# Kernel optimization log

Measured on AMD Instinct MI355X. Metric: run time of the kernel, lower is better.

Reference implementation:

```python
import jax, jax.numpy as jnp
import numpy as np

NUM_LAYERS = 3


def setup_inputs() -> dict:
    key = jax.random.key(0)
    ks = jax.random.split(key, 12)
    N, E, D_IN, D, ED = 50000, 800000, 6, 64, 4
    return {
        "x": jax.random.normal(ks[0], (N, D_IN), dtype=jnp.float32),
        "edge_index": jax.random.randint(ks[1], (2, E), 0, N, dtype=jnp.int64),
        "edge_attr": jax.random.normal(ks[2], (E, ED), dtype=jnp.float32),
        "z_soft": jax.random.uniform(ks[3], (E, ED), dtype=jnp.float32),
        "W_nt": jax.random.normal(ks[4], (D, D_IN), dtype=jnp.float32) * 0.1,
        "b_nt": jax.random.normal(ks[5], (D,), dtype=jnp.float32) * 0.1,
        "weight": jax.random.normal(ks[6], (NUM_LAYERS, D, D), dtype=jnp.float32) * 0.1,
        "W_ih": jax.random.normal(ks[7], (3 * D, D), dtype=jnp.float32) * 0.1,
        "W_hh": jax.random.normal(ks[8], (3 * D, D), dtype=jnp.float32) * 0.1,
        "b_ih": jax.random.normal(ks[9], (3 * D,), dtype=jnp.float32) * 0.1,
        "b_hh": jax.random.normal(ks[10], (3 * D,), dtype=jnp.float32) * 0.1,
    }


def gru_cell(m, h, W_ih, W_hh, b_ih, b_hh):
    # PyTorch GRUCell: gates ordered (r, z, n)
    gi = m @ W_ih.T + b_ih
    gh = h @ W_hh.T + b_hh
    i_r, i_z, i_n = jnp.split(gi, 3, axis=-1)
    h_r, h_z, h_n = jnp.split(gh, 3, axis=-1)
    r = jax.nn.sigmoid(i_r + h_r)
    z = jax.nn.sigmoid(i_z + h_z)
    n = jnp.tanh(i_n + r * h_n)
    return (1.0 - z) * n + z * h


def reference(x, edge_index, edge_attr, z_soft, W_nt, b_nt, weight, W_ih, W_hh, b_ih, b_hh):
    # node_transform: Linear + ReLU
    h = jax.nn.relu(x @ W_nt.T + b_nt)  # [N, D]
    # edge_attr gating (faithful to source; unused since edge_weight=None)
    _ = z_soft * edge_attr
    src, dst = edge_index[0], edge_index[1]
    N = h.shape[0]
    for i in range(NUM_LAYERS):
        m = h @ weight[i]                                   # [N, D]
        agg = jax.ops.segment_sum(m[src], dst, num_segments=N)  # gather-scatter add
        h = gru_cell(agg, h, W_ih, W_hh, b_ih, b_hh)
    return h
```

## Files before the change

kernel.cpp:

```cpp
#include <hip/hip_runtime.h>
#include <hip/hip_bf16.h>
#include <stdint.h>

#define D 64
typedef __hip_bfloat16 bf16;
typedef unsigned short u16;
typedef __attribute__((ext_vector_type(8))) short bf16x8;
typedef __attribute__((ext_vector_type(4))) float f32x4;

__device__ __forceinline__ float bf2f(u16 u) { return __uint_as_float(((uint32_t)u) << 16); }
__device__ __forceinline__ u16 f2bf(float f) { return __bfloat16_as_ushort(__float2bfloat16(f)); }

template <bool F32>
__device__ __forceinline__ float ld(const void* p, int i) {
    if constexpr (F32) return ((const float*)p)[i];
    else return bf2f(((const u16*)p)[i]);
}

__global__ __launch_bounds__(256) void detect_kernel(const void* x, const int* ei, int* flags) {
    __shared__ float smax[256];
    __shared__ int sor[256];
    int t = threadIdx.x;
    const u16* xs = (const u16*)x;
    float mx = 0.f;
#pragma unroll
    for (int i = 0; i < 16; ++i) {
        float a = fabsf(bf2f(xs[t * 16 + i]));
        if (!(a == a)) a = 1e30f;
        mx = fmaxf(mx, a);
    }
    int any = 0;
#pragma unroll
    for (int i = 0; i < 8; ++i) any |= ei[2 * (t * 8 + i) + 1];
    smax[t] = mx; sor[t] = any;
    __syncthreads();
    for (int s = 128; s > 0; s >>= 1) {
        if (t < s) { smax[t] = fmaxf(smax[t], smax[t + s]); sor[t] |= sor[t + s]; }
        __syncthreads();
    }
    if (t == 0) { flags[0] = (smax[0] > 1000.f) ? 1 : 0; flags[1] = (sor[0] != 0) ? 1 : 0; }
}

#define N_WCT 36864
#define N_WTH 12288
#define N_B   384
template <bool F32>
__device__ __forceinline__ void nt_body(const void* x, const void* Wnt, const void* bnt,
                                        u16* ht, int N, int blk) {
    int gid = blk * 256 + threadIdx.x;
    if (gid >= N * D) return;
    int n = gid >> 6, c = gid & 63;
    float acc = ld<F32>(bnt, c);
#pragma unroll
    for (int k = 0; k < 6; ++k)
        acc = fmaf(ld<F32>(x, n * 6 + k), ld<F32>(Wnt, c * 6 + k), acc);
    ht[gid] = f2bf(fmaxf(acc, 0.f));
}
template <bool F32>
__device__ __forceinline__ void wc_body(const void* W, const void* Wih, const void* Whh,
                                        const void* bih, const void* bhh,
                                        u16* WCh, u16* WCl, u16* WVh, u16* WVl,
                                        float* B, int blk) {
    int i = blk * 256 + threadIdx.x;
    if (i < N_WCT) {
        int l = i / 12288, rem = i % 12288, k = rem / 192, r = rem % 192;
        float acc = 0.f;
#pragma unroll 8
        for (int j = 0; j < 64; ++j)
            acc = fmaf(ld<F32>(W, l * 4096 + k * 64 + j), ld<F32>(Wih, r * 64 + j), acc);
        u16 hi = f2bf(acc);
        WCh[l * 12288 + r * 64 + k] = hi;
        WCl[l * 12288 + r * 64 + k] = f2bf(acc - bf2f(hi));
    } else if (i < N_WCT + N_WTH) {
        int rem = i - N_WCT;
        int k = rem / 192, r = rem % 192;
        float v = ld<F32>(Whh, r * 64 + k);
        u16 hi = f2bf(v);
        WVh[r * 64 + k] = hi;
        WVl[r * 64 + k] = f2bf(v - bf2f(hi));
    } else if (i < N_WCT + N_WTH + N_B) {
        int rem = i - N_WCT - N_WTH;
        B[rem] = (rem < 192) ? ld<F32>(bih, rem) : ld<F32>(bhh, rem - 192);
    }
}
__global__ __launch_bounds__(256) void prep_all(const int* __restrict__ flags,
                                                const void* x, const void* Wnt, const void* bnt,
                                                const void* W, const void* Wih, const void* Whh,
                                                const void* bih, const void* bhh,
                                                u16* ht, u16* WCh, u16* WCl, u16* WVh, u16* WVl,
                                                float* B,
                                                const int* __restrict__ ei, int* __restrict__ cnt,
                                                u16* __restrict__ ss16, int* __restrict__ novf,
                                                int* __restrict__ ovf,
                                                int E, int N, int NT_BLK, int WC_BLK) {
    int b = blockIdx.x;
    if (b < NT_BLK) {
        if (flags[0]) nt_body<true>(x, Wnt, bnt, ht, N, b);
        else          nt_body<false>(x, Wnt, bnt, ht, N, b);
    } else if (b < NT_BLK + WC_BLK) {
        if (flags[0]) wc_body<true>(W, Wih, Whh, bih, bhh, WCh, WCl, WVh, WVl, B, b - NT_BLK);
        else          wc_body<false>(W, Wih, Whh, bih, bhh, WCh, WCl, WVh, WVl, B, b - NT_BLK);
    } else {
        int i = (b - NT_BLK - WC_BLK) * 256 + threadIdx.x;
        if (i >= E) return;
        int src, dst;
        if (flags[1]) { src = ei[i];     dst = ei[E + i]; }
        else          { src = ei[2 * i]; dst = ei[2 * (E + i)]; }
        if ((unsigned)src >= (unsigned)N || (unsigned)dst >= (unsigned)N) return;
        int pos = atomicAdd(&cnt[dst], 1);
        if (pos < 64) ss16[(size_t)dst * 64 + pos] = (u16)src;
        else { int o = atomicAdd(novf, 1); ovf[2 * o] = dst; ovf[2 * o + 1] = src; }
    }
}

#define NPB 16
#define LSTR 68
__global__ __launch_bounds__(256) void layer_fused(const int* __restrict__ flags,
                                                   const u16* __restrict__ ht,
                                                   const int* __restrict__ cnt,
                                                   const u16* __restrict__ ss16,
                                                   const int* __restrict__ novf,
                                                   const int* __restrict__ ovf,
                                                   const u16* __restrict__ WCh,
                                                   const u16* __restrict__ WCl,
                                                   const u16* __restrict__ WVh,
                                                   const u16* __restrict__ WVl,
                                                   const float* __restrict__ B,
                                                   u16* __restrict__ houtb,
                                                   void* __restrict__ dout,
                                                   int N) {
    __shared__ alignas(16) float LA[NPB * LSTR];
    __shared__ alignas(16) float LH[NPB * LSTR];
    __shared__ alignas(16) u16 Ahi[NPB * 64];
    __shared__ alignas(16) u16 Alo[NPB * 64];
    __shared__ alignas(16) u16 Hb[NPB * 64];
    int t = threadIdx.x;
    int n0 = blockIdx.x * NPB;
    int lane = t & 63;
    int w = t >> 6;
    int w4 = w * 4;

    {
        if (t < 128) {
            int row = t >> 3, c = (t & 7) * 8;
            bool v = (n0 + row) < N;
            uint4 vh = make_uint4(0u, 0u, 0u, 0u);
            if (v) vh = *(const uint4*)(ht + (size_t)(n0 + row) * D + c);
            float4 f0, f1;
            f0.x = bf2f((u16)(vh.x & 0xffff)); f0.y = bf2f((u16)(vh.x >> 16));
            f0.z = bf2f((u16)(vh.y & 0xffff)); f0.w = bf2f((u16)(vh.y >> 16));
            f1.x = bf2f((u16)(vh.z & 0xffff)); f1.y = bf2f((u16)(vh.z >> 16));
            f1.z = bf2f((u16)(vh.w & 0xffff)); f1.w = bf2f((u16)(vh.w >> 16));
            *(float4*)&LH[row * LSTR + c]     = f0;
            *(float4*)&LH[row * LSTR + c + 4] = f1;
            *(uint4*)((char*)Hb + row * 128 + ((c * 2) ^ ((row & 7) << 4))) = vh;
        }
    }

    int dg[4]; int iv[4];
#pragma unroll
    for (int p = 0; p < 4; ++p) {
        int n = n0 + w4 + p;
        dg[p] = 0; iv[p] = 0;
        if (n < N) {
            int c = cnt[n]; dg[p] = (c > 64) ? 64 : c;
            iv[p] = (int)ss16[(size_t)n * 64 + lane];
        }
    }
#pragma unroll
    for (int p = 0; p < 4; ++p) {
        float acc = 0.f;
        int dgp = dg[p], ivp = iv[p];
        int j = 0;
        for (; j + 15 < dgp; j += 16) {
            int ix[16]; float a[16];
#pragma unroll
            for (int q = 0; q < 16; ++q) ix[q] = __shfl(ivp, j + q);
#pragma unroll
            for (int q = 0; q < 16; ++q) a[q] = bf2f(ht[(size_t)ix[q] * D + lane]);
            acc += (((a[0] + a[1]) + (a[2] + a[3])) + ((a[4] + a[5]) + (a[6] + a[7])))
                 + (((a[8] + a[9]) + (a[10] + a[11])) + ((a[12] + a[13]) + (a[14] + a[15])));
        }
        for (; j + 7 < dgp; j += 8) {
            int ix[8]; float a[8];
#pragma unroll
            for (int q = 0; q < 8; ++q) ix[q] = __shfl(ivp, j + q);
#pragma unroll
            for (int q = 0; q < 8; ++q) a[q] = bf2f(ht[(size_t)ix[q] * D + lane]);
            acc += ((a[0] + a[1]) + (a[2] + a[3])) + ((a[4] + a[5]) + (a[6] + a[7]));
        }
        for (; j + 3 < dgp; j += 4) {
            int ix[4]; float a[4];
#pragma unroll
            for (int q = 0; q < 4; ++q) ix[q] = __shfl(ivp, j + q);
#pragma unroll
            for (int q = 0; q < 4; ++q) a[q] = bf2f(ht[(size_t)ix[q] * D + lane]);
            acc += (a[0] + a[1]) + (a[2] + a[3]);
        }
        for (; j < dgp; ++j) acc += bf2f(ht[(size_t)__shfl(ivp, j) * D + lane]);
        LA[(w4 + p) * LSTR + lane] = acc;
    }
    __syncthreads();
    {
        int nv = novf[0];
        if (nv > 0) {
            for (int o = w; o < nv; o += 4) {
                int dst = ovf[2 * o];
                if (dst >= n0 && dst < n0 + NPB) {
                    int src = ovf[2 * o + 1];
                    atomicAdd(&LA[(dst - n0) * LSTR + lane], bf2f(ht[(size_t)src * D + lane]));
                }
            }
        }
    }
    __syncthreads();
    {
        int row = t >> 4, c = (t & 15) * 4;
        float4 v = *(const float4*)&LA[row * LSTR + c];
        u16 h0 = f2bf(v.x), h1 = f2bf(v.y), h2 = f2bf(v.z), h3 = f2bf(v.w);
        uint2 hh, ll;
        hh.x = (uint32_t)h0 | ((uint32_t)h1 << 16);
        hh.y = (uint32_t)h2 | ((uint32_t)h3 << 16);
        ll.x = (uint32_t)f2bf(v.x - bf2f(h0)) | ((uint32_t)f2bf(v.y - bf2f(h1)) << 16);
        ll.y = (uint32_t)f2bf(v.z - bf2f(h2)) | ((uint32_t)f2bf(v.w - bf2f(h3)) << 16);
        int off = row * 128 + ((c * 2) ^ ((row & 7) << 4));
        *(uint2*)((char*)Ahi + off) = hh;
        *(uint2*)((char*)Alo + off) = ll;
    }
    __syncthreads();

    int r = lane & 15, g = lane >> 4;
    int aoff0 = r * 128 + (((g * 16) + 0) ^ ((r & 7) << 4));
    int aoff1 = r * 128 + (((g * 16) + 64) ^ ((r & 7) << 4));
    bf16x8 aH0 = *(const bf16x8*)((const char*)Ahi + aoff0);
    bf16x8 aH1 = *(const bf16x8*)((const char*)Ahi + aoff1);
    bf16x8 aL0 = *(const bf16x8*)((const char*)Alo + aoff0);
    bf16x8 aL1 = *(const bf16x8*)((const char*)Alo + aoff1);
    bf16x8 hB0 = *(const bf16x8*)((const char*)Hb + aoff0);
    bf16x8 hB1 = *(const bf16x8*)((const char*)Hb + aoff1);

#define WFRAG(P, nt, ks) (*(const bf16x8*)((const char*)(P) + ((nt) * 16 + r) * 128 + (ks) * 64 + g * 16))
#define DO_TILE(nt, ai, ah) { \
    bf16x8 wch0 = WFRAG(WCh, nt, 0), wch1 = WFRAG(WCh, nt, 1); \
    bf16x8 wcl0 = WFRAG(WCl, nt, 0), wcl1 = WFRAG(WCl, nt, 1); \
    bf16x8 wvh0 = WFRAG(WVh, nt, 0), wvh1 = WFRAG(WVh, nt, 1); \
    bf16x8 wvl0 = WFRAG(WVl, nt, 0), wvl1 = WFRAG(WVl, nt, 1); \
    ai = __builtin_amdgcn_mfma_f32_16x16x32_bf16(aH0, wch0, ai, 0, 0, 0); \
    ai = __builtin_amdgcn_mfma_f32_16x16x32_bf16(aH1, wch1, ai, 0, 0, 0); \
    ai = __builtin_amdgcn_mfma_f32_16x16x32_bf16(aL0, wch0, ai, 0, 0, 0); \
    ai = __builtin_amdgcn_mfma_f32_16x16x32_bf16(aL1, wch1, ai, 0, 0, 0); \
    ai = __builtin_amdgcn_mfma_f32_16x16x32_bf16(aH0, wcl0, ai, 0, 0, 0); \
    ai = __builtin_amdgcn_mfma_f32_16x16x32_bf16(aH1, wcl1, ai, 0, 0, 0); \
    ah = __builtin_amdgcn_mfma_f32_16x16x32_bf16(hB0, wvh0, ah, 0, 0, 0); \
    ah = __builtin_amdgcn_mfma_f32_16x16x32_bf16(hB1, wvh1, ah, 0, 0, 0); \
    ah = __builtin_amdgcn_mfma_f32_16x16x32_bf16(hB0, wvl0, ah, 0, 0, 0); \
    ah = __builtin_amdgcn_mfma_f32_16x16x32_bf16(hB1, wvl1, ah, 0, 0, 0); }

    f32x4 air = {0.f, 0.f, 0.f, 0.f}, aiz = air, ain = air;
    f32x4 ahr = air, ahz = air, ahn = air;
    DO_TILE(w, air, ahr);
    DO_TILE(w + 4, aiz, ahz);
    DO_TILE(w + 8, ain, ahn);

    {
        int ch = w * 16 + r;
        float br = B[ch] + B[192 + ch];
        float bz = B[64 + ch] + B[256 + ch];
        float bi = B[128 + ch];
        float bh = B[320 + ch];
        int nb = g * 4;
#pragma unroll
        for (int j = 0; j < 4; ++j) {
            float gr = air[j] + ahr[j] + br;
            float gz = aiz[j] + ahz[j] + bz;
            float rr = 1.f / (1.f + __expf(-gr));
            float zz = 1.f / (1.f + __expf(-gz));
            float nx = ain[j] + bi + rr * (ahn[j] + bh);
            float th = 1.f - 2.f / (1.f + __expf(2.f * nx));
            float hold = LH[(nb + j) * LSTR + ch];
            LA[(nb + j) * LSTR + ch] = (1.f - zz) * th + zz * hold;
        }
    }
    __syncthreads();
    if (t < 128) {
        int row = t >> 3, c = (t & 7) * 8;
        int n = n0 + row;
        if (n < N) {
            float4 v0 = *(const float4*)&LA[row * LSTR + c];
            float4 v1 = *(const float4*)&LA[row * LSTR + c + 4];
            size_t idx = (size_t)n * D + c;
            if (houtb || !flags[0]) {
                uint4 o;
                o.x = (uint32_t)f2bf(v0.x) | ((uint32_t)f2bf(v0.y) << 16);
                o.y = (uint32_t)f2bf(v0.z) | ((uint32_t)f2bf(v0.w) << 16);
                o.z = (uint32_t)f2bf(v1.x) | ((uint32_t)f2bf(v1.y) << 16);
                o.w = (uint32_t)f2bf(v1.z) | ((uint32_t)f2bf(v1.w) << 16);
                if (houtb) *(uint4*)(houtb + idx) = o;
                else       *(uint4*)((u16*)dout + idx) = o;
            } else {
                *(float4*)((float*)dout + idx)     = v0;
                *(float4*)((float*)dout + idx + 4) = v1;
            }
        }
    }
}

extern "C" void kernel_launch(void* const* d_in, const int* in_sizes, int n_in,
                              void* d_out, int out_size, void* d_ws, size_t ws_size,
                              hipStream_t stream) {
    const void* x   = d_in[0];
    const int*  ei  = (const int*)d_in[1];
    const void* Wnt = d_in[4];
    const void* bnt = d_in[5];
    const void* Wt  = d_in[6];
    const void* Wih = d_in[7];
    const void* Whh = d_in[8];
    const void* bih = d_in[9];
    const void* bhh = d_in[10];

    int N = in_sizes[0] / 6;
    int E = in_sizes[1] / 2;
    int ND = N * D;

    int* flags = (int*)d_ws;
    float* B   = (float*)((char*)d_ws + 256);
    u16* WCh = (u16*)(B + N_B);
    u16* WCl = WCh + N_WCT;
    u16* WVh = WCl + N_WCT;
    u16* WVl = WVh + N_WTH;
    u16* htA = WVl + N_WTH;
    u16* htB = htA + ND;
    int* cnt  = (int*)(htB + ND);
    int* novf = cnt + N;
    u16* ss16 = (u16*)(novf + 1);
    int* ovf  = (int*)(ss16 + (size_t)N * 64);

    int NT_BLK = (ND + 255) / 256;
    int WC_BLK = (N_WCT + N_WTH + N_B + 255) / 256;
    int FI_BLK = (E + 255) / 256;

    hipMemsetAsync(cnt, 0, (size_t)(N + 1) * sizeof(int), stream);
    detect_kernel<<<1, 256, 0, stream>>>(x, ei, flags);
    prep_all<<<NT_BLK + WC_BLK + FI_BLK, 256, 0, stream>>>(flags, x, Wnt, bnt, Wt, Wih, Whh,
                                                           bih, bhh, htA, WCh, WCl, WVh, WVl, B,
                                                           ei, cnt, ss16, novf, ovf,
                                                           E, N, NT_BLK, WC_BLK);

    u16* hcur = htA;
    u16* hnxt = htB;
    for (int layer = 0; layer < 3; ++layer) {
        bool last = (layer == 2);
        layer_fused<<<(N + NPB - 1) / NPB, 256, 0, stream>>>(flags, hcur, cnt, ss16, novf, ovf,
                                                             WCh + layer * 12288, WCl + layer * 12288,
                                                             WVh, WVl, B,
                                                             last ? nullptr : hnxt,
                                                             last ? d_out : nullptr, N);
        u16* t = hcur; hcur = hnxt; hnxt = t;
    }
}
```

Before: 345.2 us.

## Pack edges to 32-bit, shard CSR fill by dst, branchless fixed gather

Adds a conversion kernel that packs each edge's src and dst into a single 32-bit word, with invalid edges marked. The CSR fill then reads the packed edges and uses eight dst-sharded passes so that atomics and ss16 writes from one block stay within a narrow dst range. The per-node gather becomes a fixed 16-wide predicated load for all four nodes at once, followed by a tail, and the layer kernel gains a launch-bounds occupancy hint of 3. The costs are an extra kernel, eight-fold re-reads of the packed edge array, and wasted loads on low-degree nodes.

Result: faster. 313.4 us (-9.2%).

```diff
diff --git a/kernel.cpp b/kernel.cpp
--- a/kernel.cpp
+++ b/kernel.cpp
@@ -39,6 +39,26 @@
         __syncthreads();
     }
     if (t == 0) { flags[0] = (smax[0] > 1000.f) ? 1 : 0; flags[1] = (sor[0] != 0) ? 1 : 0; }
+}
+
+__global__ __launch_bounds__(256) void convert_edges(const int* __restrict__ flags,
+                                                     const int* __restrict__ ei,
+                                                     uint32_t* __restrict__ pe, int E, int N) {
+    int i0 = blockIdx.x * 1024 + threadIdx.x;
+    bool i32 = flags[1] != 0;
+#pragma unroll
+    for (int u = 0; u < 4; ++u) {
+        int i = i0 + u * 256;
+        if (i < E) {
+            int src, dst;
+            if (i32) { src = ei[i];     dst = ei[E + i]; }
+            else     { src = ei[2 * i]; dst = ei[2 * (E + i)]; }
+            uint32_t v;
+            if ((unsigned)src >= (unsigned)N || (unsigned)dst >= (unsigned)N) v = 0xFFFFFFFFu;
+            else v = (uint32_t)(u16)src | ((uint32_t)dst << 16);
+            pe[i] = v;
+        }
+    }
 }
 
 #define N_WCT 36864
@@ -89,10 +109,11 @@
                                                 const void* bih, const void* bhh,
                                                 u16* ht, u16* WCh, u16* WCl, u16* WVh, u16* WVl,
                                                 float* B,
-                                                const int* __restrict__ ei, int* __restrict__ cnt,
+                                                const uint32_t* __restrict__ pe,
+                                                int* __restrict__ cnt,
                                                 u16* __restrict__ ss16, int* __restrict__ novf,
                                                 int* __restrict__ ovf,
-                                                int E, int N, int NT_BLK, int WC_BLK) {
+                                                int E, int N, int NT_BLK, int WC_BLK, int EPS) {
     int b = blockIdx.x;
     if (b < NT_BLK) {
         if (flags[0]) nt_body<true>(x, Wnt, bnt, ht, N, b);
@@ -101,21 +122,40 @@
         if (flags[0]) wc_body<true>(W, Wih, Whh, bih, bhh, WCh, WCl, WVh, WVl, B, b - NT_BLK);
         else          wc_body<false>(W, Wih, Whh, bih, bhh, WCh, WCl, WVh, WVl, B, b - NT_BLK);
     } else {
-        int i = (b - NT_BLK - WC_BLK) * 256 + threadIdx.x;
-        if (i >= E) return;
-        int src, dst;
-        if (flags[1]) { src = ei[i];     dst = ei[E + i]; }
-        else          { src = ei[2 * i]; dst = ei[2 * (E + i)]; }
-        if ((unsigned)src >= (unsigned)N || (unsigned)dst >= (unsigned)N) return;
-        int pos = atomicAdd(&cnt[dst], 1);
-        if (pos < 64) ss16[(size_t)dst * 64 + pos] = (u16)src;
-        else { int o = atomicAdd(novf, 1); ovf[2 * o] = dst; ovf[2 * o + 1] = src; }
+        int bf = b - NT_BLK - WC_BLK;
+        unsigned shard = (unsigned)(b & 7);
+        int beg = (bf >> 3) * EPS;
+        int end = beg + EPS; if (end > E) end = E;
+        for (int i = beg + (int)threadIdx.x; i < end; i += 256) {
+            uint32_t e = pe[i];
+            int dst = (int)(e >> 16);
+            if ((((unsigned)dst >> 4) & 7u) != shard) continue;
+            if (dst >= N) continue;
+            int src = (int)(e & 0xffffu);
+            int pos = atomicAdd(&cnt[dst], 1);
+            if (pos < 64) ss16[(size_t)dst * 64 + pos] = (u16)src;
+            else {
+                int o = atomicAdd(novf, 1);
+                if (o < E) { ovf[2 * o] = dst; ovf[2 * o + 1] = src; }
+            }
+        }
     }
 }
 
 #define NPB 16
 #define LSTR 68
-__global__ __launch_bounds__(256) void layer_fused(const int* __restrict__ flags,
+
+#define GLOAD(A, P, J) \
+    _Pragma("unroll") for (int q = 0; q < 16; ++q) { \
+        int ix_ = __shfl(iv[P], (J) + q); \
+        bool vq_ = ((J) + q) < dg[P]; \
+        ix_ = vq_ ? ix_ : 0; \
+        float tv_ = bf2f(ht[(size_t)ix_ * D + lane]); \
+        A[q] = vq_ ? tv_ : 0.f; }
+#define GSUM(A) (((((A)[0]+(A)[1])+((A)[2]+(A)[3]))+(((A)[4]+(A)[5])+((A)[6]+(A)[7]))) \
+               + ((((A)[8]+(A)[9])+((A)[10]+(A)[11]))+(((A)[12]+(A)[13])+((A)[14]+(A)[15]))))
+
+__global__ __launch_bounds__(256, 3) void layer_fused(const int* __restrict__ flags,
                                                    const u16* __restrict__ ht,
                                                    const int* __restrict__ cnt,
                                                    const u16* __restrict__ ss16,
@@ -167,43 +207,28 @@
             iv[p] = (int)ss16[(size_t)n * 64 + lane];
         }
     }
-#pragma unroll
-    for (int p = 0; p < 4; ++p) {
-        float acc = 0.f;
-        int dgp = dg[p], ivp = iv[p];
-        int j = 0;
-        for (; j + 15 < dgp; j += 16) {
-            int ix[16]; float a[16];
-#pragma unroll
-            for (int q = 0; q < 16; ++q) ix[q] = __shfl(ivp, j + q);
-#pragma unroll
-            for (int q = 0; q < 16; ++q) a[q] = bf2f(ht[(size_t)ix[q] * D + lane]);
-            acc += (((a[0] + a[1]) + (a[2] + a[3])) + ((a[4] + a[5]) + (a[6] + a[7])))
-                 + (((a[8] + a[9]) + (a[10] + a[11])) + ((a[12] + a[13]) + (a[14] + a[15])));
-        }
-        for (; j + 7 < dgp; j += 8) {
-            int ix[8]; float a[8];
-#pragma unroll
-            for (int q = 0; q < 8; ++q) ix[q] = __shfl(ivp, j + q);
-#pragma unroll
-            for (int q = 0; q < 8; ++q) a[q] = bf2f(ht[(size_t)ix[q] * D + lane]);
-            acc += ((a[0] + a[1]) + (a[2] + a[3])) + ((a[4] + a[5]) + (a[6] + a[7]));
-        }
-        for (; j + 3 < dgp; j += 4) {
-            int ix[4]; float a[4];
-#pragma unroll
-            for (int q = 0; q < 4; ++q) ix[q] = __shfl(ivp, j + q);
-#pragma unroll
-            for (int q = 0; q < 4; ++q) a[q] = bf2f(ht[(size_t)ix[q] * D + lane]);
-            acc += (a[0] + a[1]) + (a[2] + a[3]);
-        }
-        for (; j < dgp; ++j) acc += bf2f(ht[(size_t)__shfl(ivp, j) * D + lane]);
-        LA[(w4 + p) * LSTR + lane] = acc;
-    }
+    float acc0, acc1, acc2, acc3;
+    {
+        float a0[16], a1[16], a2[16], a3[16];
+        GLOAD(a0, 0, 0) GLOAD(a1, 1, 0) GLOAD(a2, 2, 0) GLOAD(a3, 3, 0)
+        acc0 = GSUM(a0); acc1 = GSUM(a1); acc2 = GSUM(a2); acc3 = GSUM(a3);
+    }
+#define GTAIL(P, ACC) if (dg[P] > 16) { \
+        float b_[16]; \
+        GLOAD(b_, P, 16) \
+        ACC += GSUM(b_); \
+        for (int j = 32; j < dg[P]; ++j) \
+            ACC += bf2f(ht[(size_t)__shfl(iv[P], j) * D + lane]); }
+    GTAIL(0, acc0) GTAIL(1, acc1) GTAIL(2, acc2) GTAIL(3, acc3)
+    LA[(w4 + 0) * LSTR + lane] = acc0;
+    LA[(w4 + 1) * LSTR + lane] = acc1;
+    LA[(w4 + 2) * LSTR + lane] = acc2;
+    LA[(w4 + 3) * LSTR + lane] = acc3;
     __syncthreads();
     {
         int nv = novf[0];
         if (nv > 0) {
+            if (nv > (1 << 20)) nv = (1 << 20);
             for (int o = w; o < nv; o += 4) {
                 int dst = ovf[2 * o];
                 if (dst >= n0 && dst < n0 + NPB) {
@@ -218,14 +243,14 @@
         int row = t >> 4, c = (t & 15) * 4;
         float4 v = *(const float4*)&LA[row * LSTR + c];
         u16 h0 = f2bf(v.x), h1 = f2bf(v.y), h2 = f2bf(v.z), h3 = f2bf(v.w);
-        uint2 hh, ll;
+        uint2 hh, llv;
         hh.x = (uint32_t)h0 | ((uint32_t)h1 << 16);
         hh.y = (uint32_t)h2 | ((uint32_t)h3 << 16);
-        ll.x = (uint32_t)f2bf(v.x - bf2f(h0)) | ((uint32_t)f2bf(v.y - bf2f(h1)) << 16);
-        ll.y = (uint32_t)f2bf(v.z - bf2f(h2)) | ((uint32_t)f2bf(v.w - bf2f(h3)) << 16);
+        llv.x = (uint32_t)f2bf(v.x - bf2f(h0)) | ((uint32_t)f2bf(v.y - bf2f(h1)) << 16);
+        llv.y = (uint32_t)f2bf(v.z - bf2f(h2)) | ((uint32_t)f2bf(v.w - bf2f(h3)) << 16);
         int off = row * 128 + ((c * 2) ^ ((row & 7) << 4));
         *(uint2*)((char*)Ahi + off) = hh;
-        *(uint2*)((char*)Alo + off) = ll;
+        *(uint2*)((char*)Alo + off) = llv;
     }
     __syncthreads();
 
@@ -334,17 +359,22 @@
     int* novf = cnt + N;
     u16* ss16 = (u16*)(novf + 1);
     int* ovf  = (int*)(ss16 + (size_t)N * 64);
+    uint32_t* pe = (uint32_t*)(ovf + 2 * (size_t)E);
 
     int NT_BLK = (ND + 255) / 256;
     int WC_BLK = (N_WCT + N_WTH + N_B + 255) / 256;
-    int FI_BLK = (E + 255) / 256;
+    int FS = (E + 1023) / 1024;
+    int EPS = (E + FS - 1) / FS;
+    int FI_BLK = 8 * FS;
+    int CV_BLK = (E + 1023) / 1024;
 
     hipMemsetAsync(cnt, 0, (size_t)(N + 1) * sizeof(int), stream);
     detect_kernel<<<1, 256, 0, stream>>>(x, ei, flags);
+    convert_edges<<<CV_BLK, 256, 0, stream>>>(flags, ei, pe, E, N);
     prep_all<<<NT_BLK + WC_BLK + FI_BLK, 256, 0, stream>>>(flags, x, Wnt, bnt, Wt, Wih, Whh,
                                                            bih, bhh, htA, WCh, WCl, WVh, WVl, B,
-                                                           ei, cnt, ss16, novf, ovf,
-                                                           E, N, NT_BLK, WC_BLK);
+                                                           pe, cnt, ss16, novf, ovf,
+                                                           E, N, NT_BLK, WC_BLK, EPS);
 
     u16* hcur = htA;
     u16* hnxt = htB;
```
